# Optimization experiments

Measured on AMD Instinct MI355X. Metric: run time of the kernel, lower is better.

## Reference

```python
import jax, jax.numpy as jnp
import numpy as np

B, T, D, HID, NB, HH = 1024, 128, 256, 512, 64, 8
LN_EPS = 1e-5


def setup_inputs() -> dict:
    key = jax.random.key(0)
    ks = jax.random.split(key, 16)
    s = 0.02
    return {
        "context_features": jax.random.normal(ks[0], (B, T, D), jnp.float32),
        "beam_history": jax.random.randint(ks[1], (B, HH), 0, NB, jnp.int64),
        "E": jax.random.normal(ks[2], (NB, D), jnp.float32) * s,          # beam embedding
        "W_in": jax.random.normal(ks[3], (2 * D, HID), jnp.float32) * s,  # in_proj Linear
        "b_in": jnp.zeros((HID,), jnp.float32),
        "W_init": jax.random.normal(ks[4], (2 * D, HID), jnp.float32) * s,
        "b_init": jnp.zeros((HID,), jnp.float32),
        "W_ih": jax.random.normal(ks[5], (3 * HID, HID), jnp.float32) * s,  # GRUCell input weights
        "W_hh": jax.random.normal(ks[6], (3 * HID, HID), jnp.float32) * s,  # GRUCell hidden weights
        "b_ih": jnp.zeros((3 * HID,), jnp.float32),
        "b_hh": jnp.zeros((3 * HID,), jnp.float32),
        "ln_g": jnp.ones((HID,), jnp.float32),
        "ln_b": jnp.zeros((HID,), jnp.float32),
        "W_o1": jax.random.normal(ks[7], (HID + D, HID), jnp.float32) * s,
        "b_o1": jnp.zeros((HID,), jnp.float32),
        "W_o2": jax.random.normal(ks[8], (HID, NB), jnp.float32) * s,
        "b_o2": jnp.zeros((NB,), jnp.float32),
    }


def _gru_cell(x, h, W_ih, W_hh, b_ih, b_hh):
    # PyTorch nn.GRUCell semantics
    gi = x @ W_ih.T + b_ih   # (B, 3H)
    gh = h @ W_hh.T + b_hh
    i_r, i_z, i_n = jnp.split(gi, 3, axis=-1)
    h_r, h_z, h_n = jnp.split(gh, 3, axis=-1)
    r = jax.nn.sigmoid(i_r + h_r)
    z = jax.nn.sigmoid(i_z + h_z)
    n = jnp.tanh(i_n + r * h_n)
    return (1.0 - z) * n + z * h


def _layernorm(x, g, b):
    mu = jnp.mean(x, axis=-1, keepdims=True)
    var = jnp.mean(jnp.square(x - mu), axis=-1, keepdims=True)
    return (x - mu) * jax.lax.rsqrt(var + LN_EPS) * g + b


def reference(context_features, beam_history, E, W_in, b_in, W_init, b_init,
              W_ih, W_hh, b_ih, b_hh, ln_g, ln_b, W_o1, b_o1, W_o2, b_o2):
    bh = beam_history.astype(jnp.int32)
    prev_beam0 = bh[:, -1]                       # (B,)
    hist_emb = jnp.mean(E[bh], axis=1)           # (B, D)
    ctx_global = jnp.mean(context_features, axis=1)  # (B, D)
    h0 = jnp.tanh(jnp.concatenate([ctx_global, hist_emb], axis=-1) @ W_init + b_init)

    ctx_t_first = jnp.transpose(context_features, (1, 0, 2))  # (T, B, D)

    def step(carry, ctx_t):
        h, prev_beam = carry
        prev_emb = E[prev_beam]                               # (B, D)
        x = jax.nn.relu(jnp.concatenate([ctx_t, prev_emb], axis=-1) @ W_in + b_in)
        h = _gru_cell(x, h, W_ih, W_hh, b_ih, b_hh)
        h_norm = _layernorm(h, ln_g, ln_b)
        hidden = jax.nn.relu(jnp.concatenate([h_norm, ctx_t], axis=-1) @ W_o1 + b_o1)
        logits_t = hidden @ W_o2 + b_o2                       # (B, NB)
        prev_beam = jnp.argmax(logits_t, axis=-1).astype(jnp.int32)
        return (h, prev_beam), logits_t

    (_, _), logits = jax.lax.scan(step, (h0, prev_beam0), ctx_t_first)
    ar_logits = jnp.transpose(logits, (1, 0, 2))  # (B, T, NB)
    return ar_logits
```

## Files before the change

kernel.cpp:

```cpp
#include <hip/hip_runtime.h>

typedef _Float16 half8 __attribute__((ext_vector_type(8)));
typedef float f32x4 __attribute__((ext_vector_type(4)));

#define MFMA(a,b,c) __builtin_amdgcn_mfma_f32_16x16x32_f16((a),(b),(c),0,0,0)

#define PKW_BYTES ((size_t)(4*468 + 4*456)*1024)
#define OFF_ETAB  PKW_BYTES
#define OFF_H0    (OFF_ETAB + (size_t)64*512*4)
#define OFF_XPRE  (OFF_H0 + (size_t)1024*512*4)
#define OFF_HPRE  (OFF_XPRE + (size_t)1024*128*512*2)

__device__ __forceinline__ void gll16(const void* g, void* l){
  __builtin_amdgcn_global_load_lds(
      (const __attribute__((address_space(1))) void*)g,
      (__attribute__((address_space(3))) void*)l, 16, 0, 0);
}

__global__ void packw_k(const float* __restrict__ W_ih, const float* __restrict__ W_hh,
                        const float* __restrict__ W_o1, const float* __restrict__ W_o2,
                        _Float16* __restrict__ pkw)
{
  int ts = blockIdx.x, w = blockIdx.y;
  if (w >= 4 && ts >= 456) return;
  int lane = threadIdx.x, lo = lane & 15, kb8 = (lane >> 4)*8;
  half8 v;
  #pragma unroll
  for (int e = 0; e < 8; e++) v[e] = (_Float16)0.f;
  if (ts < 384){
    int i = ts/96, r = ts%96, a = r/16, kq = r%16;
    int n = w*64 + i*16 + lo;
    #pragma unroll
    for (int e = 0; e < 8; e++){
      int k = kq*32 + kb8 + e;
      v[e] = (a < 3) ? (_Float16)W_ih[(a*512 + n)*512 + k]
                     : (_Float16)W_hh[((a-3)*512 + n)*512 + k];
    }
  } else if (ts < 448){
    int td = ts - 384;
    int i = td >> 4, ks = td & 15, n = w*64 + i*16 + lo;
    #pragma unroll
    for (int e = 0; e < 8; e++) v[e] = (_Float16)W_o1[(ks*32 + kb8 + e)*512 + n];
  } else if (ts >= 448 && ts < 464 && w < 4){
    int te = ts - 448, n = w*16 + lo;
    #pragma unroll
    for (int e = 0; e < 8; e++) v[e] = (_Float16)W_o2[(te*32 + kb8 + e)*64 + n];
  }
  long base = (w < 4) ? (long)w*468 : (long)1872 + (long)(w-4)*456;
  *(half8*)(pkw + (base + ts)*512 + lane*8) = v;
}

__global__ void etab_k(const float* __restrict__ E, const float* __restrict__ W_in,
                       const float* __restrict__ b_in, float* __restrict__ Etab)
{
  int e = blockIdx.x, tid = threadIdx.x;
  __shared__ float er[256];
  if (tid < 256) er[tid] = E[e*256 + tid];
  __syncthreads();
  for (int j = tid; j < 512; j += 256){
    float acc = b_in[j];
    for (int k = 0; k < 256; k++) acc += er[k] * W_in[(256 + k)*512 + j];
    Etab[e*512 + j] = acc;
  }
}

__global__ __launch_bounds__(512) void h0_k(const float* __restrict__ ctx,
    const int* __restrict__ bh, const float* __restrict__ E,
    const float* __restrict__ W_init, const float* __restrict__ b_init,
    float* __restrict__ h0w)
{
  int b0 = blockIdx.x * 16, tid = threadIdx.x;
  __shared__ float cat[16][512];
  int c = tid & 255, rh = tid >> 8;
  for (int rr = 0; rr < 8; rr++){
    int r2 = rh*8 + rr;
    const float* p = ctx + ((b0 + r2)*128)*256 + c;
    float acc = 0.f;
    for (int t = 0; t < 128; t++) acc += p[t*256];
    cat[r2][c] = acc * (1.f/128.f);
    float s = 0.f;
    #pragma unroll
    for (int hh = 0; hh < 8; hh++){
      int e = bh[(b0 + r2)*8 + hh];
      s += E[e*256 + c];
    }
    cat[r2][256 + c] = s * 0.125f;
  }
  __syncthreads();
  int j = tid;
  float acc[16];
  #pragma unroll
  for (int r2 = 0; r2 < 16; r2++) acc[r2] = b_init[j];
  for (int k = 0; k < 512; k++){
    float wv = W_init[k*512 + j];
    #pragma unroll
    for (int r2 = 0; r2 < 16; r2++) acc[r2] += cat[r2][k] * wv;
  }
  #pragma unroll
  for (int r2 = 0; r2 < 16; r2++) h0w[(b0 + r2)*512 + j] = tanhf(acc[r2]);
}

__global__ __launch_bounds__(512) void prep_k(const float* __restrict__ ctx,
    const float* __restrict__ W_in, const float* __restrict__ W_o1,
    _Float16* __restrict__ xpre, _Float16* __restrict__ hpre)
{
  int b = blockIdx.x, tid = threadIdx.x;
  int w = tid >> 6, lane = tid & 63, lo = lane & 15, hi = lane >> 4;
  extern __shared__ __align__(16) _Float16 A_lds[];

  {
    int ra = tid >> 2, ca = (tid & 3)*64;
    const float* p = ctx + ((long)b*128 + ra)*256 + ca;
    #pragma unroll
    for (int c8 = 0; c8 < 8; c8++){
      float4 f0 = *(const float4*)(p + c8*8);
      float4 f1 = *(const float4*)(p + c8*8 + 4);
      half8 v;
      v[0]=(_Float16)f0.x; v[1]=(_Float16)f0.y; v[2]=(_Float16)f0.z; v[3]=(_Float16)f0.w;
      v[4]=(_Float16)f1.x; v[5]=(_Float16)f1.y; v[6]=(_Float16)f1.z; v[7]=(_Float16)f1.w;
      *(half8*)((char*)A_lds + (((ra*512 + (ca + c8*8)*2)) ^ ((ra&7)<<4))) = v;
    }
  }
  __syncthreads();

  const float* Wb = (w < 4) ? W_in : (W_o1 + 512*512);
  _Float16* outp = (w < 4) ? xpre : hpre;
  const int colbase = (w & 3)*128;
  const int aswzp = (lo & 7) << 4;

  #pragma unroll 1
  for (int cth = 0; cth < 4; cth++){
    half8 bf0[8], bf1[8];
    const int n0 = colbase + cth*32 + lo;
    #pragma unroll
    for (int ks = 0; ks < 8; ks++){
      const int kb = ks*32 + hi*8;
      half8 v0, v1;
      #pragma unroll
      for (int e = 0; e < 8; e++){
        v0[e] = (_Float16)Wb[(kb + e)*512 + n0];
        v1[e] = (_Float16)Wb[(kb + e)*512 + n0 + 16];
      }
      bf0[ks] = v0; bf1[ks] = v1;
    }
    #pragma unroll 1
    for (int rt = 0; rt < 8; rt++){
      f32x4 acc0 = {0,0,0,0}, acc1 = {0,0,0,0};
      #pragma unroll
      for (int ks = 0; ks < 8; ks++){
        half8 a = *(const half8*)((const char*)A_lds +
                   ((((rt*16 + lo)*512 + hi*16 + ks*64)) ^ aswzp));
        acc0 = MFMA(a, bf0[ks], acc0);
        acc1 = MFMA(a, bf1[ks], acc1);
      }
      #pragma unroll
      for (int rr = 0; rr < 4; rr++){
        int t = rt*16 + hi*4 + rr;
        long rowoff = ((long)b*128 + t)*512 + colbase + cth*32;
        outp[rowoff +      lo] = (_Float16)acc0[rr];
        outp[rowoff + 16 + lo] = (_Float16)acc1[rr];
      }
    }
  }
}

#define AFRAG(buf, base, ks) (*(const half8*)((const char*)(buf) + ((((base) + (ks)*64)) ^ aswz)))
#define WSTORE(buf, row, j, val) \
  *(_Float16*)((char*)(buf) + ((((row)*1024 + (j)*2)) ^ ((((row)&7))<<4))) = (_Float16)(val)
#define WSTORE8(buf, row, colf16, v8) \
  *(half8*)((char*)(buf) + ((((row)*1024 + (colf16)*2)) ^ ((((row)&7))<<4))) = (v8)

#define VMW8 do{ asm volatile("s_waitcnt vmcnt(8)" ::: "memory"); \
                 __builtin_amdgcn_sched_barrier(0); }while(0)

#define ISSUE4(c_, sl_) do{ \
    int cw_ = (c_); if (cw_ >= 96) cw_ -= 96; \
    const char* s_ = pkw_w + (((long)cw_)<<12) + (lane<<4); \
    char* d_ = ring + ((((sl_)*8) + w)<<12); \
    gll16(s_,        d_); \
    gll16(s_ + 1024, d_ + 1024); \
    gll16(s_ + 2048, d_ + 2048); \
    gll16(s_ + 3072, d_ + 3072); \
    __builtin_amdgcn_sched_barrier(0); \
  }while(0)

#define RFR4(sl_, q_) (*(const half8*)(ring + ((((sl_)*8) + w)<<12) + ((q_)<<10) + (lane<<4)))

__global__ __launch_bounds__(512) void main8_k(
    const _Float16* __restrict__ pkw, const float* __restrict__ Etab,
    const float* __restrict__ h0w, const _Float16* __restrict__ xpre,
    const _Float16* __restrict__ hpre, const int* __restrict__ bh,
    const float* __restrict__ b_ih, const float* __restrict__ b_hh,
    const float* __restrict__ lng, const float* __restrict__ lnb,
    const float* __restrict__ b_o1, const float* __restrict__ b_o2,
    float* __restrict__ out)
{
  const int g = blockIdx.x, tid = threadIdx.x;
  const int w = tid >> 6, lane = tid & 63, lo = lane & 15, hi = lane >> 4;
  const int r0 = g*16;

  extern __shared__ __align__(16) char smem[];
  char*      ring = smem;
  _Float16*  h_s  = (_Float16*)(smem + 98304);
  _Float16*  hn_s = (_Float16*)(smem + 114688);
  _Float16*  xh_s = (_Float16*)(smem + 131072);
  float*     lg_s = (float*)(smem + 147456);
  float*     stats= (float*)(smem + 151552);
  float*     murs = (float*)(smem + 152576);
  int*       pb   = (int*)(smem + 152704);

  float bcr[4], bcz[4], bin_[4], bhn[4], bo1v[4], lngv[4], lnbv[4];
  #pragma unroll
  for (int i = 0; i < 4; i++){
    int j = w*64 + i*16 + lo;
    bcr[i] = b_ih[j]     + b_hh[j];
    bcz[i] = b_ih[512+j] + b_hh[512+j];
    bin_[i]= b_ih[1024+j];
    bhn[i] = b_hh[1024+j];
    bo1v[i]= b_o1[j]; lngv[i]= lng[j]; lnbv[i]= lnb[j];
  }
  const float bo2v = (w < 4) ? b_o2[w*16 + lo] : 0.f;

  float hreg[4][4];
  #pragma unroll
  for (int i = 0; i < 4; i++)
    #pragma unroll
    for (int rr = 0; rr < 4; rr++)
      hreg[i][rr] = h0w[(r0 + hi*4 + rr)*512 + w*64 + i*16 + lo];

  #pragma unroll
  for (int c2 = 0; c2 < 2; c2++){
    int ch = tid*2 + c2, rr = ch >> 6, c8 = ch & 63;
    const float* p = h0w + (r0 + rr)*512 + c8*8;
    half8 v;
    #pragma unroll
    for (int e = 0; e < 8; e++) v[e] = (_Float16)p[e];
    *(half8*)((char*)h_s + (((rr*1024 + c8*16)) ^ ((rr&7)<<4))) = v;
  }
  if (tid < 16) pb[tid] = bh[(r0 + tid)*8 + 7];

  const int aswz  = (lo & 7) << 4;
  const int abase = lo*1024 + hi*16;
  const char* pkw_w = (const char*)pkw +
      ((w < 4) ? (long)w*468*1024 : ((long)1872 + (long)(w-4)*456)*1024);

  ISSUE4(0, 0);
  ISSUE4(1, 1);
  __syncthreads();

  #pragma unroll 1
  for (int t = 0; t < 128; t++){
    {
      int rowA = tid >> 5, c32 = (tid & 31)*16;
      const _Float16* xp = xpre + (((long)(r0 + rowA)*128 + t)*512) + c32;
      half8 x0 = __builtin_nontemporal_load((const half8*)xp);
      half8 x1 = __builtin_nontemporal_load((const half8*)(xp + 8));
      const float* ep = Etab + pb[rowA]*512 + c32;
      float4 e0 = *(const float4*)(ep);
      float4 e1 = *(const float4*)(ep + 4);
      float4 e2 = *(const float4*)(ep + 8);
      float4 e3 = *(const float4*)(ep + 12);
      half8 o0, o1;
      o0[0]=(_Float16)fmaxf((float)x0[0]+e0.x,0.f); o0[1]=(_Float16)fmaxf((float)x0[1]+e0.y,0.f);
      o0[2]=(_Float16)fmaxf((float)x0[2]+e0.z,0.f); o0[3]=(_Float16)fmaxf((float)x0[3]+e0.w,0.f);
      o0[4]=(_Float16)fmaxf((float)x0[4]+e1.x,0.f); o0[5]=(_Float16)fmaxf((float)x0[5]+e1.y,0.f);
      o0[6]=(_Float16)fmaxf((float)x0[6]+e1.z,0.f); o0[7]=(_Float16)fmaxf((float)x0[7]+e1.w,0.f);
      o1[0]=(_Float16)fmaxf((float)x1[0]+e2.x,0.f); o1[1]=(_Float16)fmaxf((float)x1[1]+e2.y,0.f);
      o1[2]=(_Float16)fmaxf((float)x1[2]+e2.z,0.f); o1[3]=(_Float16)fmaxf((float)x1[3]+e2.w,0.f);
      o1[4]=(_Float16)fmaxf((float)x1[4]+e3.x,0.f); o1[5]=(_Float16)fmaxf((float)x1[5]+e3.y,0.f);
      o1[6]=(_Float16)fmaxf((float)x1[6]+e3.z,0.f); o1[7]=(_Float16)fmaxf((float)x1[7]+e3.w,0.f);
      WSTORE8(xh_s, rowA, c32,     o0);
      WSTORE8(xh_s, rowA, c32 + 8, o1);
    }
    __syncthreads();

    float srow[4] = {0,0,0,0}, sqrow[4] = {0,0,0,0};
    #pragma unroll 1
    for (int i = 0; i < 4; i++){
      f32x4 a0={0,0,0,0},a1={0,0,0,0},a2={0,0,0,0},a3={0,0,0,0},a4={0,0,0,0},a5={0,0,0,0};
      #pragma unroll
      for (int a6 = 0; a6 < 6; a6++){
        #pragma unroll
        for (int cq = 0; cq < 4; cq++){
          const int pidx = i*24 + a6*4 + cq;
          ISSUE4(pidx + 2, (a6*4 + cq + 2) % 3);
          VMW8;
          #pragma unroll
          for (int q = 0; q < 4; q++){
            half8 af = AFRAG((a6 < 3) ? xh_s : h_s, abase, cq*4 + q);
            half8 bf = RFR4((a6*4 + cq) % 3, q);
            if      (a6 == 0) a0 = MFMA(af, bf, a0);
            else if (a6 == 1) a1 = MFMA(af, bf, a1);
            else if (a6 == 2) a2 = MFMA(af, bf, a2);
            else if (a6 == 3) a3 = MFMA(af, bf, a3);
            else if (a6 == 4) a4 = MFMA(af, bf, a4);
            else              a5 = MFMA(af, bf, a5);
          }
        }
      }
      #pragma unroll
      for (int rr = 0; rr < 4; rr++){
        float rg = 1.f/(1.f + __expf(-(a0[rr] + a3[rr] + bcr[i])));
        float zg = 1.f/(1.f + __expf(-(a1[rr] + a4[rr] + bcz[i])));
        float aa = (a2[rr] + bin_[i]) + rg*(a5[rr] + bhn[i]);
        float ea = __expf(-2.f*fabsf(aa));
        float th = (1.f - ea)/(1.f + ea);
        float ng = (aa < 0.f) ? -th : th;
        float hv = (1.f - zg)*ng + zg*hreg[i][rr];
        hreg[i][rr] = hv;
        srow[rr] += hv; sqrow[rr] += hv*hv;
      }
    }
    #pragma unroll
    for (int d = 1; d < 16; d <<= 1){
      #pragma unroll
      for (int rr = 0; rr < 4; rr++){
        srow[rr]  += __shfl_xor(srow[rr],  d);
        sqrow[rr] += __shfl_xor(sqrow[rr], d);
      }
    }
    if (lo == 0){
      #pragma unroll
      for (int rr = 0; rr < 4; rr++){
        stats[((w*4 + hi)*4 + rr)*2 + 0] = srow[rr];
        stats[((w*4 + hi)*4 + rr)*2 + 1] = sqrow[rr];
      }
    }
    __syncthreads();
    if (w == 0 && lane < 16){
      float s = 0.f, q = 0.f;
      #pragma unroll
      for (int ww = 0; ww < 8; ww++){
        s += stats[((ww*4 + (lane>>2))*4 + (lane&3))*2 + 0];
        q += stats[((ww*4 + (lane>>2))*4 + (lane&3))*2 + 1];
      }
      float mu = s*(1.f/512.f);
      float var = q*(1.f/512.f) - mu*mu;
      murs[lane*2 + 0] = mu;
      murs[lane*2 + 1] = rsqrtf(var + 1e-5f);
    }
    __syncthreads();

    float hp[4][4];
    #pragma unroll
    for (int rr = 0; rr < 4; rr++){
      int row = hi*4 + rr;
      float mu = murs[row*2 + 0], rs = murs[row*2 + 1];
      #pragma unroll
      for (int i = 0; i < 4; i++){
        int jc = w*64 + i*16 + lo;
        float hv = hreg[i][rr];
        WSTORE(h_s,  row, jc, hv);
        WSTORE(hn_s, row, jc, (hv - mu)*rs*lngv[i] + lnbv[i]);
        hp[i][rr] = (float)__builtin_nontemporal_load(
            &hpre[(((long)(r0 + row)*128 + t)*512) + jc]);
      }
    }
    __syncthreads();

    #pragma unroll 1
    for (int i = 0; i < 4; i++){
      half8 bd[16];
      #pragma unroll
      for (int ks = 0; ks < 16; ks++)
        bd[ks] = *(const half8*)(pkw_w + (((long)(384 + i*16 + ks)) << 10) + (lane << 4));
      f32x4 dacc = {0,0,0,0};
      #pragma unroll
      for (int ks = 0; ks < 16; ks++)
        dacc = MFMA(AFRAG(hn_s, abase, ks), bd[ks], dacc);
      #pragma unroll
      for (int rr = 0; rr < 4; rr++){
        int row = hi*4 + rr;
        WSTORE(xh_s, row, w*64 + i*16 + lo, fmaxf(dacc[rr] + bo1v[i] + hp[i][rr], 0.f));
      }
    }
    __syncthreads();

    if (w < 4){
      half8 be[16];
      #pragma unroll
      for (int ks = 0; ks < 16; ks++)
        be[ks] = *(const half8*)(pkw_w + (((long)(448 + ks)) << 10) + (lane << 4));
      f32x4 eacc = {0,0,0,0};
      #pragma unroll
      for (int ks = 0; ks < 16; ks++)
        eacc = MFMA(AFRAG(xh_s, abase, ks), be[ks], eacc);
      #pragma unroll
      for (int rr = 0; rr < 4; rr++){
        int row = hi*4 + rr;
        lg_s[row*64 + w*16 + lo] = eacc[rr] + bo2v;
      }
    }
    __syncthreads();

    #pragma unroll
    for (int sub = 0; sub < 2; sub++){
      int r2 = w*2 + sub;
      float v = lg_s[r2*64 + lane];
      __builtin_nontemporal_store(v, &out[(((long)(r0 + r2))*128 + t)*64 + lane]);
      int idx = lane;
      #pragma unroll
      for (int d = 1; d < 64; d <<= 1){
        float ov = __shfl_xor(v, d);
        int oi = __shfl_xor(idx, d);
        if (ov > v || (ov == v && oi < idx)){ v = ov; idx = oi; }
      }
      if (lane == 0) pb[r2] = idx;
    }
    __syncthreads();
  }
}

extern "C" void kernel_launch(void* const* d_in, const int* in_sizes, int n_in,
                              void* d_out, int out_size, void* d_ws, size_t ws_size,
                              hipStream_t stream)
{
  const float* ctx    = (const float*)d_in[0];
  const int*   bh     = (const int*)d_in[1];
  const float* E      = (const float*)d_in[2];
  const float* W_in   = (const float*)d_in[3];
  const float* b_in   = (const float*)d_in[4];
  const float* W_init = (const float*)d_in[5];
  const float* b_init = (const float*)d_in[6];
  const float* W_ih   = (const float*)d_in[7];
  const float* W_hh   = (const float*)d_in[8];
  const float* b_ih   = (const float*)d_in[9];
  const float* b_hh   = (const float*)d_in[10];
  const float* ln_g   = (const float*)d_in[11];
  const float* ln_b   = (const float*)d_in[12];
  const float* W_o1   = (const float*)d_in[13];
  const float* b_o1   = (const float*)d_in[14];
  const float* W_o2   = (const float*)d_in[15];
  const float* b_o2   = (const float*)d_in[16];
  float* out = (float*)d_out;

  _Float16* pkw  = (_Float16*)d_ws;
  float*    Etab = (float*)((char*)d_ws + OFF_ETAB);
  float*    h0w  = (float*)((char*)d_ws + OFF_H0);
  _Float16* xpre = (_Float16*)((char*)d_ws + OFF_XPRE);
  _Float16* hpre = (_Float16*)((char*)d_ws + OFF_HPRE);

  (void)hipFuncSetAttribute((const void*)prep_k,
      hipFuncAttributeMaxDynamicSharedMemorySize, 65536);
  (void)hipFuncSetAttribute((const void*)main8_k,
      hipFuncAttributeMaxDynamicSharedMemorySize, 152768);

  hipLaunchKernelGGL(packw_k, dim3(468, 8), dim3(64), 0, stream, W_ih, W_hh, W_o1, W_o2, pkw);
  hipLaunchKernelGGL(etab_k, dim3(64), dim3(256), 0, stream, E, W_in, b_in, Etab);
  hipLaunchKernelGGL(h0_k, dim3(64), dim3(512), 0, stream, ctx, bh, E, W_init, b_init, h0w);
  hipLaunchKernelGGL(prep_k, dim3(1024), dim3(512), 65536, stream, ctx, W_in, W_o1, xpre, hpre);
  hipLaunchKernelGGL(main8_k, dim3(64), dim3(512), 152768, stream,
                     pkw, Etab, h0w, xpre, hpre, bh,
                     b_ih, b_hh, ln_g, ln_b, b_o1, b_o2, out);
}
```

Baseline: 5.570 ms.

## Replace LDS ring prefetch of GRU weights with direct register loads

Removes the triple-buffered global_load_lds ring and its explicit vmcnt waits. The GRU weight tiles are now loaded straight into registers in batches of eight fragments before each MFMA group. Shared memory shrinks from about 150KB to static arrays, and o1/layernorm parameters move from registers into LDS to cut register pressure. The aim is to drop the LDS round trip and waitcnt stalls, at the cost of less explicit latency hiding for the weight stream. There is only one 64-block wave, so the smaller LDS footprint does not add occupancy.

```diff
diff --git a/kernel.cpp b/kernel.cpp
--- a/kernel.cpp
+++ b/kernel.cpp
@@ -10,12 +10,6 @@
 #define OFF_H0    (OFF_ETAB + (size_t)64*512*4)
 #define OFF_XPRE  (OFF_H0 + (size_t)1024*512*4)
 #define OFF_HPRE  (OFF_XPRE + (size_t)1024*128*512*2)
-
-__device__ __forceinline__ void gll16(const void* g, void* l){
-  __builtin_amdgcn_global_load_lds(
-      (const __attribute__((address_space(1))) void*)g,
-      (__attribute__((address_space(3))) void*)l, 16, 0, 0);
-}
 
 __global__ void packw_k(const float* __restrict__ W_ih, const float* __restrict__ W_hh,
                         const float* __restrict__ W_o1, const float* __restrict__ W_o2,
@@ -170,23 +164,7 @@
 #define WSTORE8(buf, row, colf16, v8) \
   *(half8*)((char*)(buf) + ((((row)*1024 + (colf16)*2)) ^ ((((row)&7))<<4))) = (v8)
 
-#define VMW8 do{ asm volatile("s_waitcnt vmcnt(8)" ::: "memory"); \
-                 __builtin_amdgcn_sched_barrier(0); }while(0)
-
-#define ISSUE4(c_, sl_) do{ \
-    int cw_ = (c_); if (cw_ >= 96) cw_ -= 96; \
-    const char* s_ = pkw_w + (((long)cw_)<<12) + (lane<<4); \
-    char* d_ = ring + ((((sl_)*8) + w)<<12); \
-    gll16(s_,        d_); \
-    gll16(s_ + 1024, d_ + 1024); \
-    gll16(s_ + 2048, d_ + 2048); \
-    gll16(s_ + 3072, d_ + 3072); \
-    __builtin_amdgcn_sched_barrier(0); \
-  }while(0)
-
-#define RFR4(sl_, q_) (*(const half8*)(ring + ((((sl_)*8) + w)<<12) + ((q_)<<10) + (lane<<4)))
-
-__global__ __launch_bounds__(512) void main8_k(
+__global__ __launch_bounds__(512) void main10_k(
     const _Float16* __restrict__ pkw, const float* __restrict__ Etab,
     const float* __restrict__ h0w, const _Float16* __restrict__ xpre,
     const _Float16* __restrict__ hpre, const int* __restrict__ bh,
@@ -199,17 +177,16 @@
   const int w = tid >> 6, lane = tid & 63, lo = lane & 15, hi = lane >> 4;
   const int r0 = g*16;
 
-  extern __shared__ __align__(16) char smem[];
-  char*      ring = smem;
-  _Float16*  h_s  = (_Float16*)(smem + 98304);
-  _Float16*  hn_s = (_Float16*)(smem + 114688);
-  _Float16*  xh_s = (_Float16*)(smem + 131072);
-  float*     lg_s = (float*)(smem + 147456);
-  float*     stats= (float*)(smem + 151552);
-  float*     murs = (float*)(smem + 152576);
-  int*       pb   = (int*)(smem + 152704);
-
-  float bcr[4], bcz[4], bin_[4], bhn[4], bo1v[4], lngv[4], lnbv[4];
+  __shared__ __align__(16) _Float16 h_s [16*512];
+  __shared__ __align__(16) _Float16 hn_s[16*512];
+  __shared__ __align__(16) _Float16 xh_s[16*512];
+  __shared__ float lg_s[16*64];
+  __shared__ float stats[8][4][4][2];
+  __shared__ float murs[16][2];
+  __shared__ float bias_s[3][512];
+  __shared__ int   pb[16];
+
+  float bcr[4], bcz[4], bin_[4], bhn[4];
   #pragma unroll
   for (int i = 0; i < 4; i++){
     int j = w*64 + i*16 + lo;
@@ -217,9 +194,13 @@
     bcz[i] = b_ih[512+j] + b_hh[512+j];
     bin_[i]= b_ih[1024+j];
     bhn[i] = b_hh[1024+j];
-    bo1v[i]= b_o1[j]; lngv[i]= lng[j]; lnbv[i]= lnb[j];
   }
   const float bo2v = (w < 4) ? b_o2[w*16 + lo] : 0.f;
+  if (tid < 512){
+    bias_s[0][tid] = b_o1[tid];
+    bias_s[1][tid] = lng[tid];
+    bias_s[2][tid] = lnb[tid];
+  }
 
   float hreg[4][4];
   #pragma unroll
@@ -238,15 +219,12 @@
     *(half8*)((char*)h_s + (((rr*1024 + c8*16)) ^ ((rr&7)<<4))) = v;
   }
   if (tid < 16) pb[tid] = bh[(r0 + tid)*8 + 7];
+  __syncthreads();
 
   const int aswz  = (lo & 7) << 4;
   const int abase = lo*1024 + hi*16;
   const char* pkw_w = (const char*)pkw +
       ((w < 4) ? (long)w*468*1024 : ((long)1872 + (long)(w-4)*456)*1024);
-
-  ISSUE4(0, 0);
-  ISSUE4(1, 1);
-  __syncthreads();
 
   #pragma unroll 1
   for (int t = 0; t < 128; t++){
@@ -280,21 +258,23 @@
       f32x4 a0={0,0,0,0},a1={0,0,0,0},a2={0,0,0,0},a3={0,0,0,0},a4={0,0,0,0},a5={0,0,0,0};
       #pragma unroll
       for (int a6 = 0; a6 < 6; a6++){
+        const _Float16* ab = (a6 < 3) ? xh_s : h_s;
         #pragma unroll
-        for (int cq = 0; cq < 4; cq++){
-          const int pidx = i*24 + a6*4 + cq;
-          ISSUE4(pidx + 2, (a6*4 + cq + 2) % 3);
-          VMW8;
+        for (int hf = 0; hf < 2; hf++){
+          half8 bb[8];
+          const char* tp = pkw_w + (((long)(i*96 + a6*16 + hf*8)) << 10) + (lane << 4);
           #pragma unroll
-          for (int q = 0; q < 4; q++){
-            half8 af = AFRAG((a6 < 3) ? xh_s : h_s, abase, cq*4 + q);
-            half8 bf = RFR4((a6*4 + cq) % 3, q);
-            if      (a6 == 0) a0 = MFMA(af, bf, a0);
-            else if (a6 == 1) a1 = MFMA(af, bf, a1);
-            else if (a6 == 2) a2 = MFMA(af, bf, a2);
-            else if (a6 == 3) a3 = MFMA(af, bf, a3);
-            else if (a6 == 4) a4 = MFMA(af, bf, a4);
-            else              a5 = MFMA(af, bf, a5);
+          for (int k8 = 0; k8 < 8; k8++)
+            bb[k8] = *(const half8*)(tp + ((long)k8 << 10));
+          #pragma unroll
+          for (int k8 = 0; k8 < 8; k8++){
+            half8 af = AFRAG(ab, abase, hf*8 + k8);
+            if      (a6 == 0) a0 = MFMA(af, bb[k8], a0);
+            else if (a6 == 1) a1 = MFMA(af, bb[k8], a1);
+            else if (a6 == 2) a2 = MFMA(af, bb[k8], a2);
+            else if (a6 == 3) a3 = MFMA(af, bb[k8], a3);
+            else if (a6 == 4) a4 = MFMA(af, bb[k8], a4);
+            else              a5 = MFMA(af, bb[k8], a5);
           }
         }
       }
@@ -322,8 +302,8 @@
     if (lo == 0){
       #pragma unroll
       for (int rr = 0; rr < 4; rr++){
-        stats[((w*4 + hi)*4 + rr)*2 + 0] = srow[rr];
-        stats[((w*4 + hi)*4 + rr)*2 + 1] = sqrow[rr];
+        stats[w][hi][rr][0] = srow[rr];
+        stats[w][hi][rr][1] = sqrow[rr];
       }
     }
     __syncthreads();
@@ -331,13 +311,13 @@
       float s = 0.f, q = 0.f;
       #pragma unroll
       for (int ww = 0; ww < 8; ww++){
-        s += stats[((ww*4 + (lane>>2))*4 + (lane&3))*2 + 0];
-        q += stats[((ww*4 + (lane>>2))*4 + (lane&3))*2 + 1];
+        s += stats[ww][lane>>2][lane&3][0];
+        q += stats[ww][lane>>2][lane&3][1];
       }
       float mu = s*(1.f/512.f);
       float var = q*(1.f/512.f) - mu*mu;
-      murs[lane*2 + 0] = mu;
-      murs[lane*2 + 1] = rsqrtf(var + 1e-5f);
+      murs[lane][0] = mu;
+      murs[lane][1] = rsqrtf(var + 1e-5f);
     }
     __syncthreads();
 
@@ -345,13 +325,13 @@
     #pragma unroll
     for (int rr = 0; rr < 4; rr++){
       int row = hi*4 + rr;
-      float mu = murs[row*2 + 0], rs = murs[row*2 + 1];
+      float mu = murs[row][0], rs = murs[row][1];
       #pragma unroll
       for (int i = 0; i < 4; i++){
         int jc = w*64 + i*16 + lo;
         float hv = hreg[i][rr];
         WSTORE(h_s,  row, jc, hv);
-        WSTORE(hn_s, row, jc, (hv - mu)*rs*lngv[i] + lnbv[i]);
+        WSTORE(hn_s, row, jc, (hv - mu)*rs*bias_s[1][jc] + bias_s[2][jc]);
         hp[i][rr] = (float)__builtin_nontemporal_load(
             &hpre[(((long)(r0 + row)*128 + t)*512) + jc]);
       }
@@ -368,10 +348,11 @@
       #pragma unroll
       for (int ks = 0; ks < 16; ks++)
         dacc = MFMA(AFRAG(hn_s, abase, ks), bd[ks], dacc);
+      const float bo1j = bias_s[0][w*64 + i*16 + lo];
       #pragma unroll
       for (int rr = 0; rr < 4; rr++){
         int row = hi*4 + rr;
-        WSTORE(xh_s, row, w*64 + i*16 + lo, fmaxf(dacc[rr] + bo1v[i] + hp[i][rr], 0.f));
+        WSTORE(xh_s, row, w*64 + i*16 + lo, fmaxf(dacc[rr] + bo1j + hp[i][rr], 0.f));
       }
     }
     __syncthreads();
@@ -442,14 +423,12 @@
 
   (void)hipFuncSetAttribute((const void*)prep_k,
       hipFuncAttributeMaxDynamicSharedMemorySize, 65536);
-  (void)hipFuncSetAttribute((const void*)main8_k,
-      hipFuncAttributeMaxDynamicSharedMemorySize, 152768);
 
   hipLaunchKernelGGL(packw_k, dim3(468, 8), dim3(64), 0, stream, W_ih, W_hh, W_o1, W_o2, pkw);
   hipLaunchKernelGGL(etab_k, dim3(64), dim3(256), 0, stream, E, W_in, b_in, Etab);
   hipLaunchKernelGGL(h0_k, dim3(64), dim3(512), 0, stream, ctx, bh, E, W_init, b_init, h0w);
   hipLaunchKernelGGL(prep_k, dim3(1024), dim3(512), 65536, stream, ctx, W_in, W_o1, xpre, hpre);
-  hipLaunchKernelGGL(main8_k, dim3(64), dim3(512), 152768, stream,
+  hipLaunchKernelGGL(main10_k, dim3(64), dim3(512), 0, stream,
                      pkw, Etab, h0w, xpre, hpre, bh,
                      b_ih, b_hh, ln_g, ln_b, b_o1, b_o2, out);
 }
```

Result: slower. 6.284 ms (+12.8%).

## Split GRU weight streaming: LDS ring for half the waves, direct loads for rest

Applied to the files above, without the earlier changes.

Only waves 0-3 now stream their GRU weight chunks through the LDS ring via global_load_lds. Waves 4-7 instead load their B fragments directly from global memory into registers in batches of eight. This halves the ring size and frees LDS, and the LayerNorm gamma/beta and b_o1 biases move from registers into LDS to relieve register pressure. The two wave groups now follow different load paths, which risks load imbalance, more global-load latency for the direct-load waves, and extra register use for the bb buffers.

```diff
diff --git a/kernel.cpp b/kernel.cpp
--- a/kernel.cpp
+++ b/kernel.cpp
@@ -176,7 +176,7 @@
 #define ISSUE4(c_, sl_) do{ \
     int cw_ = (c_); if (cw_ >= 96) cw_ -= 96; \
     const char* s_ = pkw_w + (((long)cw_)<<12) + (lane<<4); \
-    char* d_ = ring + ((((sl_)*8) + w)<<12); \
+    char* d_ = ring + ((((sl_)*4) + w)<<12); \
     gll16(s_,        d_); \
     gll16(s_ + 1024, d_ + 1024); \
     gll16(s_ + 2048, d_ + 2048); \
@@ -184,9 +184,9 @@
     __builtin_amdgcn_sched_barrier(0); \
   }while(0)
 
-#define RFR4(sl_, q_) (*(const half8*)(ring + ((((sl_)*8) + w)<<12) + ((q_)<<10) + (lane<<4)))
-
-__global__ __launch_bounds__(512) void main8_k(
+#define RFR4(sl_, q_) (*(const half8*)(ring + ((((sl_)*4) + w)<<12) + ((q_)<<10) + (lane<<4)))
+
+__global__ __launch_bounds__(512) void main11_k(
     const _Float16* __restrict__ pkw, const float* __restrict__ Etab,
     const float* __restrict__ h0w, const _Float16* __restrict__ xpre,
     const _Float16* __restrict__ hpre, const int* __restrict__ bh,
@@ -200,16 +200,17 @@
   const int r0 = g*16;
 
   extern __shared__ __align__(16) char smem[];
-  char*      ring = smem;
-  _Float16*  h_s  = (_Float16*)(smem + 98304);
-  _Float16*  hn_s = (_Float16*)(smem + 114688);
-  _Float16*  xh_s = (_Float16*)(smem + 131072);
-  float*     lg_s = (float*)(smem + 147456);
-  float*     stats= (float*)(smem + 151552);
-  float*     murs = (float*)(smem + 152576);
-  int*       pb   = (int*)(smem + 152704);
-
-  float bcr[4], bcz[4], bin_[4], bhn[4], bo1v[4], lngv[4], lnbv[4];
+  char*      ring  = smem;
+  _Float16*  h_s   = (_Float16*)(smem + 49152);
+  _Float16*  hn_s  = (_Float16*)(smem + 65536);
+  _Float16*  xh_s  = (_Float16*)(smem + 81920);
+  float*     lg_s  = (float*)(smem + 98304);
+  float*     stats = (float*)(smem + 102400);
+  float*     murs  = (float*)(smem + 103424);
+  int*       pb    = (int*)(smem + 103552);
+  float*     bias_s= (float*)(smem + 103616);
+
+  float bcr[4], bcz[4], bin_[4], bhn[4];
   #pragma unroll
   for (int i = 0; i < 4; i++){
     int j = w*64 + i*16 + lo;
@@ -217,9 +218,11 @@
     bcz[i] = b_ih[512+j] + b_hh[512+j];
     bin_[i]= b_ih[1024+j];
     bhn[i] = b_hh[1024+j];
-    bo1v[i]= b_o1[j]; lngv[i]= lng[j]; lnbv[i]= lnb[j];
   }
   const float bo2v = (w < 4) ? b_o2[w*16 + lo] : 0.f;
+  bias_s[0*512 + tid] = b_o1[tid];
+  bias_s[1*512 + tid] = lng[tid];
+  bias_s[2*512 + tid] = lnb[tid];
 
   float hreg[4][4];
   #pragma unroll
@@ -244,8 +247,7 @@
   const char* pkw_w = (const char*)pkw +
       ((w < 4) ? (long)w*468*1024 : ((long)1872 + (long)(w-4)*456)*1024);
 
-  ISSUE4(0, 0);
-  ISSUE4(1, 1);
+  if (w < 4){ ISSUE4(0, 0); ISSUE4(1, 1); }
   __syncthreads();
 
   #pragma unroll 1
@@ -275,40 +277,81 @@
     __syncthreads();
 
     float srow[4] = {0,0,0,0}, sqrow[4] = {0,0,0,0};
-    #pragma unroll 1
-    for (int i = 0; i < 4; i++){
-      f32x4 a0={0,0,0,0},a1={0,0,0,0},a2={0,0,0,0},a3={0,0,0,0},a4={0,0,0,0},a5={0,0,0,0};
-      #pragma unroll
-      for (int a6 = 0; a6 < 6; a6++){
+    if (w < 4){
+      #pragma unroll 1
+      for (int i = 0; i < 4; i++){
+        f32x4 a0={0,0,0,0},a1={0,0,0,0},a2={0,0,0,0},a3={0,0,0,0},a4={0,0,0,0},a5={0,0,0,0};
         #pragma unroll
-        for (int cq = 0; cq < 4; cq++){
-          const int pidx = i*24 + a6*4 + cq;
-          ISSUE4(pidx + 2, (a6*4 + cq + 2) % 3);
-          VMW8;
+        for (int a6 = 0; a6 < 6; a6++){
           #pragma unroll
-          for (int q = 0; q < 4; q++){
-            half8 af = AFRAG((a6 < 3) ? xh_s : h_s, abase, cq*4 + q);
-            half8 bf = RFR4((a6*4 + cq) % 3, q);
-            if      (a6 == 0) a0 = MFMA(af, bf, a0);
-            else if (a6 == 1) a1 = MFMA(af, bf, a1);
-            else if (a6 == 2) a2 = MFMA(af, bf, a2);
-            else if (a6 == 3) a3 = MFMA(af, bf, a3);
-            else if (a6 == 4) a4 = MFMA(af, bf, a4);
-            else              a5 = MFMA(af, bf, a5);
+          for (int cq = 0; cq < 4; cq++){
+            const int pidx = i*24 + a6*4 + cq;
+            ISSUE4(pidx + 2, (a6*4 + cq + 2) % 3);
+            VMW8;
+            #pragma unroll
+            for (int q = 0; q < 4; q++){
+              half8 af = AFRAG((a6 < 3) ? xh_s : h_s, abase, cq*4 + q);
+              half8 bf = RFR4((a6*4 + cq) % 3, q);
+              if      (a6 == 0) a0 = MFMA(af, bf, a0);
+              else if (a6 == 1) a1 = MFMA(af, bf, a1);
+              else if (a6 == 2) a2 = MFMA(af, bf, a2);
+              else if (a6 == 3) a3 = MFMA(af, bf, a3);
+              else if (a6 == 4) a4 = MFMA(af, bf, a4);
+              else              a5 = MFMA(af, bf, a5);
+            }
           }
         }
-      }
-      #pragma unroll
-      for (int rr = 0; rr < 4; rr++){
-        float rg = 1.f/(1.f + __expf(-(a0[rr] + a3[rr] + bcr[i])));
-        float zg = 1.f/(1.f + __expf(-(a1[rr] + a4[rr] + bcz[i])));
-        float aa = (a2[rr] + bin_[i]) + rg*(a5[rr] + bhn[i]);
-        float ea = __expf(-2.f*fabsf(aa));
-        float th = (1.f - ea)/(1.f + ea);
-        float ng = (aa < 0.f) ? -th : th;
-        float hv = (1.f - zg)*ng + zg*hreg[i][rr];
-        hreg[i][rr] = hv;
-        srow[rr] += hv; sqrow[rr] += hv*hv;
+        #pragma unroll
+        for (int rr = 0; rr < 4; rr++){
+          float rg = 1.f/(1.f + __expf(-(a0[rr] + a3[rr] + bcr[i])));
+          float zg = 1.f/(1.f + __expf(-(a1[rr] + a4[rr] + bcz[i])));
+          float aa = (a2[rr] + bin_[i]) + rg*(a5[rr] + bhn[i]);
+          float ea = __expf(-2.f*fabsf(aa));
+          float th = (1.f - ea)/(1.f + ea);
+          float ng = (aa < 0.f) ? -th : th;
+          float hv = (1.f - zg)*ng + zg*hreg[i][rr];
+          hreg[i][rr] = hv;
+          srow[rr] += hv; sqrow[rr] += hv*hv;
+        }
+      }
+    } else {
+      #pragma unroll 1
+      for (int i = 0; i < 4; i++){
+        f32x4 a0={0,0,0,0},a1={0,0,0,0},a2={0,0,0,0},a3={0,0,0,0},a4={0,0,0,0},a5={0,0,0,0};
+        #pragma unroll
+        for (int a6 = 0; a6 < 6; a6++){
+          const _Float16* ab = (a6 < 3) ? xh_s : h_s;
+          #pragma unroll
+          for (int hf = 0; hf < 2; hf++){
+            half8 bb[8];
+            const char* tp = pkw_w + (((long)(i*96 + a6*16 + hf*8)) << 10) + (lane << 4);
+            #pragma unroll
+            for (int k8 = 0; k8 < 8; k8++)
+              bb[k8] = *(const half8*)(tp + ((long)k8 << 10));
+            #pragma unroll
+            for (int k8 = 0; k8 < 8; k8++){
+              half8 af = AFRAG(ab, abase, hf*8 + k8);
+              if      (a6 == 0) a0 = MFMA(af, bb[k8], a0);
+              else if (a6 == 1) a1 = MFMA(af, bb[k8], a1);
+              else if (a6 == 2) a2 = MFMA(af, bb[k8], a2);
+              else if (a6 == 3) a3 = MFMA(af, bb[k8], a3);
+              else if (a6 == 4) a4 = MFMA(af, bb[k8], a4);
+              else              a5 = MFMA(af, bb[k8], a5);
+            }
+          }
+        }
+        #pragma unroll
+        for (int rr = 0; rr < 4; rr++){
+          float rg = 1.f/(1.f + __expf(-(a0[rr] + a3[rr] + bcr[i])));
+          float zg = 1.f/(1.f + __expf(-(a1[rr] + a4[rr] + bcz[i])));
+          float aa = (a2[rr] + bin_[i]) + rg*(a5[rr] + bhn[i]);
+          float ea = __expf(-2.f*fabsf(aa));
+          float th = (1.f - ea)/(1.f + ea);
+          float ng = (aa < 0.f) ? -th : th;
+          float hv = (1.f - zg)*ng + zg*hreg[i][rr];
+          hreg[i][rr] = hv;
+          srow[rr] += hv; sqrow[rr] += hv*hv;
+        }
       }
     }
     #pragma unroll
@@ -351,7 +394,7 @@
         int jc = w*64 + i*16 + lo;
         float hv = hreg[i][rr];
         WSTORE(h_s,  row, jc, hv);
-        WSTORE(hn_s, row, jc, (hv - mu)*rs*lngv[i] + lnbv[i]);
+        WSTORE(hn_s, row, jc, (hv - mu)*rs*bias_s[512 + jc] + bias_s[1024 + jc]);
         hp[i][rr] = (float)__builtin_nontemporal_load(
             &hpre[(((long)(r0 + row)*128 + t)*512) + jc]);
       }
@@ -368,10 +411,11 @@
       #pragma unroll
       for (int ks = 0; ks < 16; ks++)
         dacc = MFMA(AFRAG(hn_s, abase, ks), bd[ks], dacc);
+      const float bo1j = bias_s[w*64 + i*16 + lo];
       #pragma unroll
       for (int rr = 0; rr < 4; rr++){
         int row = hi*4 + rr;
-        WSTORE(xh_s, row, w*64 + i*16 + lo, fmaxf(dacc[rr] + bo1v[i] + hp[i][rr], 0.f));
+        WSTORE(xh_s, row, w*64 + i*16 + lo, fmaxf(dacc[rr] + bo1j + hp[i][rr], 0.f));
       }
     }
     __syncthreads();
@@ -442,14 +486,14 @@
 
   (void)hipFuncSetAttribute((const void*)prep_k,
       hipFuncAttributeMaxDynamicSharedMemorySize, 65536);
-  (void)hipFuncSetAttribute((const void*)main8_k,
-      hipFuncAttributeMaxDynamicSharedMemorySize, 152768);
+  (void)hipFuncSetAttribute((const void*)main11_k,
+      hipFuncAttributeMaxDynamicSharedMemorySize, 110592);
 
   hipLaunchKernelGGL(packw_k, dim3(468, 8), dim3(64), 0, stream, W_ih, W_hh, W_o1, W_o2, pkw);
   hipLaunchKernelGGL(etab_k, dim3(64), dim3(256), 0, stream, E, W_in, b_in, Etab);
   hipLaunchKernelGGL(h0_k, dim3(64), dim3(512), 0, stream, ctx, bh, E, W_init, b_init, h0w);
   hipLaunchKernelGGL(prep_k, dim3(1024), dim3(512), 65536, stream, ctx, W_in, W_o1, xpre, hpre);
-  hipLaunchKernelGGL(main8_k, dim3(64), dim3(512), 152768, stream,
+  hipLaunchKernelGGL(main11_k, dim3(64), dim3(512), 110592, stream,
                      pkw, Etab, h0w, xpre, hpre, bh,
                      b_ih, b_hh, ln_g, ln_b, b_o1, b_o2, out);
 }
```

New measurement: 5.720 ms. 1.03x slower.
